# Kernel optimization log

Hardware: AMD Instinct MI355X
Metric: run time of the kernel (lower is better)

The kernel has to match this reference:

```python
import jax, jax.numpy as jnp
import numpy as np

NUM_HEADS = 16
HEAD_DIM = 128
HIDDEN = NUM_HEADS * HEAD_DIM


def rotate_half(x):
    x1, x2 = jnp.split(x, 2, axis=-1)
    return jnp.concatenate((-x2, x1), axis=-1)


def setup_inputs() -> dict:
    key = jax.random.key(0)
    ks = jax.random.split(key, 7)
    b, s = 2, 2048
    return {
        "hidden_states": jax.random.normal(ks[0], (b, s, HIDDEN), dtype=jnp.float32),
        "cos": jax.random.normal(ks[1], (1, 1, s, HEAD_DIM), dtype=jnp.float32),
        "sin": jax.random.normal(ks[2], (1, 1, s, HEAD_DIM), dtype=jnp.float32),
        "Wq": jax.random.normal(ks[3], (HIDDEN, HIDDEN), dtype=jnp.float32) * 0.02,
        "Wk": jax.random.normal(ks[4], (HIDDEN, HIDDEN), dtype=jnp.float32) * 0.02,
        "Wv": jax.random.normal(ks[5], (HIDDEN, HIDDEN), dtype=jnp.float32) * 0.02,
        "Wo": jax.random.normal(ks[6], (HIDDEN, HIDDEN), dtype=jnp.float32) * 0.02,
    }


def reference(hidden_states, cos, sin, Wq, Wk, Wv, Wo):
    b, s, _ = hidden_states.shape

    def proj(W):
        # [b,s,hidden] -> [b,H,s,D]
        return (hidden_states @ W).reshape(b, s, NUM_HEADS, HEAD_DIM).transpose(0, 2, 1, 3)

    q = proj(Wq)
    k = proj(Wk)
    v = proj(Wv)

    # RoPE: cos/sin [1,1,s,D] broadcast over batch and heads
    q = q * cos + rotate_half(q) * sin
    k = k * cos + rotate_half(k) * sin

    scale = 1.0 / jnp.sqrt(jnp.asarray(HEAD_DIM, dtype=q.dtype))
    scores = jnp.einsum("bhqd,bhkd->bhqk", q, k) * scale  # [b,H,s,s]
    attn = jax.nn.softmax(scores, axis=-1)  # no mask applied (matches source)
    out = jnp.einsum("bhqk,bhkd->bhqd", attn, v)  # [b,H,s,D]
    out = out.transpose(0, 2, 1, 3).reshape(b, s, HIDDEN)
    return out @ Wo
```

## Files before the change

### kernel.cpp

```cpp
#include <hip/hip_runtime.h>

typedef short bf16x8 __attribute__((ext_vector_type(8)));
typedef float f32x4 __attribute__((ext_vector_type(4)));

#define HID   2048
#define S_LEN 2048
#define NH    16
#define HD    128
#define BATCH 2
#define NROWS (BATCH * S_LEN)

__device__ __forceinline__ float bf2f(unsigned short u) {
    union { unsigned int i; float f; } v;
    v.i = ((unsigned int)u) << 16;
    return v.f;
}
__device__ __forceinline__ unsigned short f2bf(float f) {
    union { float f; unsigned int i; } v;
    v.f = f;
    unsigned int u = v.i;
    return (unsigned short)((u + 0x7fffu + ((u >> 16) & 1u)) >> 16);
}

__device__ __forceinline__ unsigned int pkbf(float a, float b) {
#if defined(__has_builtin) && __has_builtin(__builtin_amdgcn_cvt_pk_bf16_f32)
    typedef __bf16 bf2_t __attribute__((ext_vector_type(2)));
    bf2_t v = __builtin_amdgcn_cvt_pk_bf16_f32(a, b);
    unsigned int u;
    __builtin_memcpy(&u, &v, 4);
    return u;
#else
    return (unsigned int)f2bf(a) | ((unsigned int)f2bf(b) << 16);
#endif
}

__device__ __forceinline__ float exp2_fast(float x) {
#if defined(__has_builtin) && __has_builtin(__builtin_amdgcn_exp2f)
    return __builtin_amdgcn_exp2f(x);
#else
    return __expf(x * 0.6931471805599453f);
#endif
}

__device__ __forceinline__ void async16(const unsigned short* g, unsigned short* l) {
    __builtin_amdgcn_global_load_lds(
        (const __attribute__((address_space(1))) unsigned int*)g,
        (__attribute__((address_space(3))) unsigned int*)l, 16, 0, 0);
}

__global__ __launch_bounds__(256) void prep(const float* __restrict__ hs,
                                            const float* __restrict__ Wa,
                                            const float* __restrict__ Wb,
                                            const float* __restrict__ Wc,
                                            unsigned short* __restrict__ Xb,
                                            unsigned short* __restrict__ WT) {
    int z = blockIdx.z;
    int t = threadIdx.x;
    if (z == 3) {
        size_t idx = (((size_t)blockIdx.y * 64 + blockIdx.x) * 256 + t) * 8;
        float4 v0 = *(const float4*)(hs + idx);
        float4 v1 = *(const float4*)(hs + idx + 4);
        uint4 o;
        o.x = pkbf(v0.x, v0.y);
        o.y = pkbf(v0.z, v0.w);
        o.z = pkbf(v1.x, v1.y);
        o.w = pkbf(v1.z, v1.w);
        *(uint4*)(Xb + idx) = o;
        return;
    }
    __shared__ float tile[32][33];
    int tx = t & 31, ty = t >> 5;
    int bx = blockIdx.x, by = blockIdx.y;
    const float* W = (z == 0) ? Wa : ((z == 1) ? Wb : Wc);
    unsigned short* dst = WT + (size_t)z * HID * HID;
#pragma unroll
    for (int i = 0; i < 4; i++)
        tile[ty + i * 8][tx] = W[(size_t)(by * 32 + ty + i * 8) * HID + bx * 32 + tx];
    __syncthreads();
#pragma unroll
    for (int i = 0; i < 4; i++)
        dst[(size_t)(bx * 32 + ty + i * 8) * HID + by * 32 + tx] = f2bf(tile[tx][ty + i * 8]);
}

__global__ __launch_bounds__(256) void transpose_cast(const float* __restrict__ W,
                                                      unsigned short* __restrict__ WT) {
    __shared__ float tile[32][33];
    int t = threadIdx.x;
    int tx = t & 31, ty = t >> 5;
    int bx = blockIdx.x, by = blockIdx.y;
#pragma unroll
    for (int i = 0; i < 4; i++)
        tile[ty + i * 8][tx] = W[(size_t)(by * 32 + ty + i * 8) * HID + bx * 32 + tx];
    __syncthreads();
#pragma unroll
    for (int i = 0; i < 4; i++)
        WT[(size_t)(bx * 32 + ty + i * 8) * HID + by * 32 + tx] = f2bf(tile[tx][ty + i * 8]);
}

template <int MODE>
__global__ __launch_bounds__(256, 2) void gemm_bt(const unsigned short* __restrict__ A,
                                                  const unsigned short* __restrict__ Bt,
                                                  unsigned short* __restrict__ Qo,
                                                  unsigned short* __restrict__ Ko,
                                                  unsigned short* __restrict__ Vo,
                                                  float* __restrict__ Fo,
                                                  const float* __restrict__ cosp,
                                                  const float* __restrict__ sinp,
                                                  int n_shift) {
    __shared__ unsigned short SM[16384];
    unsigned short* Asm = SM;
    unsigned short* Bsm = SM + 8192;
    int t = threadIdx.x;
    int wave = t >> 6, lane = t & 63;
    int wm = wave >> 1, wn = wave & 1;
    int c = lane & 15, quad = lane >> 4;
    int m0 = blockIdx.y * 128, nloc = blockIdx.x * 128;

    int lr = lane >> 3;
    int cb = (lane & 7) ^ (lr & 7);
    const unsigned short* Ag = A + (size_t)(m0 + wave * 32 + lr) * HID + cb * 8;
    const unsigned short* Bg = Bt + (size_t)(nloc + wave * 32 + lr) * HID + cb * 8;
    unsigned short* Al = Asm + wave * 2048;
    unsigned short* Bl = Bsm + wave * 2048;

    f32x4 zero = {0.f, 0.f, 0.f, 0.f};
    f32x4 acc[4][4];
#pragma unroll
    for (int i = 0; i < 4; i++)
#pragma unroll
        for (int j = 0; j < 4; j++) acc[i][j] = zero;

    for (int it = 0; it < 32; it++) {
        int k0 = it * 64;
#pragma unroll
        for (int j = 0; j < 4; j++) {
            async16(Ag + k0 + j * 8 * HID, Al + j * 512);
            async16(Bg + k0 + j * 8 * HID, Bl + j * 512);
        }
        __syncthreads();
#pragma unroll
        for (int kk = 0; kk < 2; kk++) {
            bf16x8 af[4], bfr[4];
#pragma unroll
            for (int mt = 0; mt < 4; mt++)
                af[mt] = *(const bf16x8*)(Asm + (wm * 64 + mt * 16 + c) * 64 +
                                          (((kk * 4 + quad) ^ (c & 7)) * 8));
#pragma unroll
            for (int nt = 0; nt < 4; nt++)
                bfr[nt] = *(const bf16x8*)(Bsm + (wn * 64 + nt * 16 + c) * 64 +
                                           (((kk * 4 + quad) ^ (c & 7)) * 8));
#pragma unroll
            for (int mt = 0; mt < 4; mt++)
#pragma unroll
                for (int nt = 0; nt < 4; nt++)
                    acc[mt][nt] = __builtin_amdgcn_mfma_f32_16x16x32_bf16(af[mt], bfr[nt],
                                                                          acc[mt][nt], 0, 0, 0);
        }
        __syncthreads();
    }

    if (MODE == 2) {
#pragma unroll
        for (int mt = 0; mt < 4; mt++)
#pragma unroll
            for (int nt = 0; nt < 4; nt++)
#pragma unroll
                for (int r = 0; r < 4; r++) {
                    int row = m0 + wm * 64 + mt * 16 + quad * 4 + r;
                    int col = nloc + wn * 64 + nt * 16 + c;
                    Fo[(size_t)row * HID + col] = acc[mt][nt][r];
                }
    } else {
        int nglob0 = n_shift + nloc;
        int mat = nglob0 >> 11;
        int h = (nglob0 & 2047) >> 7;
        if (mat == 2) {
#pragma unroll
            for (int mt = 0; mt < 4; mt++)
#pragma unroll
                for (int nt = 0; nt < 4; nt++) {
                    int d = wn * 64 + nt * 16 + c;
                    int row0 = m0 + wm * 64 + mt * 16 + quad * 4;
                    int b = row0 >> 11, s = row0 & 2047;
                    ushort4 o;
                    o.x = f2bf(acc[mt][nt][0]);
                    o.y = f2bf(acc[mt][nt][1]);
                    o.z = f2bf(acc[mt][nt][2]);
                    o.w = f2bf(acc[mt][nt][3]);
                    *(ushort4*)(Vo + ((size_t)(b * NH + h) * HD + d) * S_LEN + s) = o;
                }
        } else {
            unsigned short* Cb = (mat == 0) ? Qo : Ko;
            float scl = (mat == 0) ? 0.12751743f : 1.0f;
            __syncthreads();
#pragma unroll
            for (int mt = 0; mt < 4; mt++)
#pragma unroll
                for (int nt = 0; nt < 4; nt++) {
                    ushort4 o;
                    o.x = f2bf(acc[mt][nt][0]);
                    o.y = f2bf(acc[mt][nt][1]);
                    o.z = f2bf(acc[mt][nt][2]);
                    o.w = f2bf(acc[mt][nt][3]);
                    *(ushort4*)(SM + (mt * 4 + nt) * 1024 + t * 4) = o;
                }
            __syncthreads();
            int partner = (wm * 2 + (wn ^ 1)) * 64 + lane;
            float sgn = wn ? 1.0f : -1.0f;
#pragma unroll
            for (int mt = 0; mt < 4; mt++) {
#pragma unroll
                for (int nt = 0; nt < 4; nt++) {
                    ushort4 pv = *(const ushort4*)(SM + (mt * 4 + nt) * 1024 + partner * 4);
                    float part[4] = {bf2f(pv.x), bf2f(pv.y), bf2f(pv.z), bf2f(pv.w)};
                    int col = wn * 64 + nt * 16 + c;
#pragma unroll
                    for (int r = 0; r < 4; r++) {
                        int row = m0 + wm * 64 + mt * 16 + quad * 4 + r;
                        int b = row >> 11, s = row & 2047;
                        float cv = cosp[s * HD + col], sv = sinp[s * HD + col];
                        float out = (acc[mt][nt][r] * cv + sgn * part[r] * sv) * scl;
                        Cb[((size_t)(b * NH + h) * S_LEN + s) * HD + col] = f2bf(out);
                    }
                }
            }
        }
    }
}

#define PKS 72
__global__ __launch_bounds__(256, 2) void attn_kernel(const unsigned short* __restrict__ Q,
                                                      const unsigned short* __restrict__ Kg,
                                                      const unsigned short* __restrict__ Vt,
                                                      unsigned short* __restrict__ Aout) {
    __shared__ unsigned short Ksm[64 * 128];
    __shared__ unsigned short Vsm[128 * 64];
    __shared__ __align__(16) unsigned short Psm[4 * 2 * 16 * PKS];
    int bh = blockIdx.y;
    int b = bh >> 4, h = bh & 15;
    int t = threadIdx.x;
    int wave = t >> 6, lane = t & 63;
    int c = lane & 15, quad = lane >> 4;
    int q0 = blockIdx.x * 128 + wave * 32;
    const unsigned short* Qp = Q + (size_t)bh * S_LEN * HD;
    const unsigned short* Kp = Kg + (size_t)bh * S_LEN * HD;
    const unsigned short* Vp = Vt + (size_t)bh * HD * S_LEN;

    bf16x8 qf[2][4];
#pragma unroll
    for (int qn = 0; qn < 2; qn++)
#pragma unroll
        for (int kk = 0; kk < 4; kk++)
            qf[qn][kk] = *(const bf16x8*)(Qp + (size_t)(q0 + qn * 16 + c) * HD + kk * 32 + quad * 8);

    f32x4 zero = {0.f, 0.f, 0.f, 0.f};
    f32x4 o_acc[2][8];
#pragma unroll
    for (int qn = 0; qn < 2; qn++)
#pragma unroll
        for (int nt = 0; nt < 8; nt++) o_acc[qn][nt] = zero;
    float lsum[2] = {0.f, 0.f};

    for (int key0 = 0; key0 < S_LEN; key0 += 64) {
#pragma unroll
        for (int j = 0; j < 4; j++) {
            int fc = (wave * 4 + j) * 64 + lane;
            int rK = fc >> 4, cbK = (fc & 15) ^ (rK & 15);
            async16(Kp + (size_t)(key0 + rK) * HD + cbK * 8, Ksm + (wave * 4 + j) * 512);
            int rV = fc >> 3, cbV = (fc & 7) ^ (rV & 7);
            async16(Vp + (size_t)rV * S_LEN + key0 + cbV * 8, Vsm + (wave * 4 + j) * 512);
        }
        __syncthreads();

        f32x4 sacc[4][2];
#pragma unroll
        for (int km = 0; km < 4; km++)
#pragma unroll
            for (int qn = 0; qn < 2; qn++) sacc[km][qn] = zero;
#pragma unroll
        for (int kk = 0; kk < 4; kk++) {
            bf16x8 kfr[4];
#pragma unroll
            for (int km = 0; km < 4; km++)
                kfr[km] = *(const bf16x8*)(Ksm + (km * 16 + c) * HD + (((kk * 4 + quad) ^ c)) * 8);
#pragma unroll
            for (int km = 0; km < 4; km++)
#pragma unroll
                for (int qn = 0; qn < 2; qn++)
                    sacc[km][qn] = __builtin_amdgcn_mfma_f32_16x16x32_bf16(kfr[km], qf[qn][kk],
                                                                           sacc[km][qn], 0, 0, 0);
        }

#pragma unroll
        for (int qn = 0; qn < 2; qn++) {
#pragma unroll
            for (int km = 0; km < 4; km++) {
                float e0 = exp2_fast(sacc[km][qn][0]);
                float e1 = exp2_fast(sacc[km][qn][1]);
                float e2 = exp2_fast(sacc[km][qn][2]);
                float e3 = exp2_fast(sacc[km][qn][3]);
                lsum[qn] += (e0 + e1) + (e2 + e3);
                uint2 pk;
                pk.x = pkbf(e0, e1);
                pk.y = pkbf(e2, e3);
                *(uint2*)(Psm + ((wave * 2 + qn) * 16 + c) * PKS + km * 16 + quad * 4) = pk;
            }
        }
        asm volatile("" ::: "memory");
        __builtin_amdgcn_s_waitcnt(0xc07f);
        asm volatile("" ::: "memory");

#pragma unroll
        for (int kf = 0; kf < 2; kf++) {
            bf16x8 pf[2];
#pragma unroll
            for (int qn = 0; qn < 2; qn++)
                pf[qn] = *(const bf16x8*)(Psm + ((wave * 2 + qn) * 16 + c) * PKS + kf * 32 + quad * 8);
#pragma unroll
            for (int nt = 0; nt < 8; nt++) {
                bf16x8 vf = *(const bf16x8*)(Vsm + (nt * 16 + c) * 64 +
                                             (((kf * 4 + quad) ^ (c & 7))) * 8);
#pragma unroll
                for (int qn = 0; qn < 2; qn++)
                    o_acc[qn][nt] = __builtin_amdgcn_mfma_f32_16x16x32_bf16(pf[qn], vf,
                                                                            o_acc[qn][nt], 0, 0, 0);
            }
        }
        __syncthreads();
    }

#pragma unroll
    for (int qn = 0; qn < 2; qn++) {
        lsum[qn] += __shfl_xor(lsum[qn], 16);
        lsum[qn] += __shfl_xor(lsum[qn], 32);
    }
    float inv[2][4];
#pragma unroll
    for (int qn = 0; qn < 2; qn++)
#pragma unroll
        for (int r = 0; r < 4; r++)
            inv[qn][r] = 1.0f / __shfl(lsum[qn], quad * 4 + r);

#pragma unroll
    for (int qn = 0; qn < 2; qn++) {
#pragma unroll
        for (int r = 0; r < 4; r++) {
            int srow = q0 + qn * 16 + quad * 4 + r;
            size_t base = ((size_t)(b * S_LEN + srow)) * HID + h * HD;
#pragma unroll
            for (int nt = 0; nt < 8; nt++)
                Aout[base + nt * 16 + c] = f2bf(o_acc[qn][nt][r] * inv[qn][r]);
        }
    }
}

extern "C" void kernel_launch(void* const* d_in, const int* in_sizes, int n_in,
                              void* d_out, int out_size, void* d_ws, size_t ws_size,
                              hipStream_t stream) {
    const float* hs   = (const float*)d_in[0];
    const float* cosp = (const float*)d_in[1];
    const float* sinp = (const float*)d_in[2];
    const float* Wq   = (const float*)d_in[3];
    const float* Wk   = (const float*)d_in[4];
    const float* Wv   = (const float*)d_in[5];
    const float* Wo   = (const float*)d_in[6];

    char* ws = (char*)d_ws;
    unsigned short* Xb = (unsigned short*)(ws);
    unsigned short* Qb = (unsigned short*)(ws + (16ull << 20));
    unsigned short* Kb = (unsigned short*)(ws + (32ull << 20));
    unsigned short* Vb = (unsigned short*)(ws + (48ull << 20));
    unsigned short* WT = (unsigned short*)(ws + (64ull << 20));

    const bool fused = ws_size >= (88ull << 20);

    if (fused) {
        prep<<<dim3(64, 64, 4), 256, 0, stream>>>(hs, Wq, Wk, Wv, Xb, WT);
        gemm_bt<0><<<dim3(48, 32), 256, 0, stream>>>(Xb, WT, Qb, Kb, Vb, nullptr,
                                                     cosp, sinp, 0);
        attn_kernel<<<dim3(16, 32), 256, 0, stream>>>(Qb, Kb, Vb, Xb );
        unsigned short* WoT = (unsigned short*)(ws + (16ull << 20));
        transpose_cast<<<dim3(64, 64), 256, 0, stream>>>(Wo, WoT);
        gemm_bt<2><<<dim3(16, 32), 256, 0, stream>>>(Xb, WoT, nullptr, nullptr, nullptr,
                                                     (float*)d_out, cosp, sinp, 0);
    } else {
        prep<<<dim3(64, 64, 1), 256, 0, stream>>>(hs, Wq, Wq, Wq, Xb, WT);
        prep<<<dim3(64, 64, 4), 256, 0, stream>>>(hs, Wq, Wq, Wq, Xb, WT);
        gemm_bt<0><<<dim3(16, 32), 256, 0, stream>>>(Xb, WT, Qb, Kb, Vb, nullptr,
                                                     cosp, sinp, 0);
        transpose_cast<<<dim3(64, 64), 256, 0, stream>>>(Wk, WT);
        gemm_bt<0><<<dim3(16, 32), 256, 0, stream>>>(Xb, WT, Qb, Kb, Vb, nullptr,
                                                     cosp, sinp, 2048);
        transpose_cast<<<dim3(64, 64), 256, 0, stream>>>(Wv, WT);
        gemm_bt<0><<<dim3(16, 32), 256, 0, stream>>>(Xb, WT, Qb, Kb, Vb, nullptr,
                                                     cosp, sinp, 4096);
        attn_kernel<<<dim3(16, 32), 256, 0, stream>>>(Qb, Kb, Vb, Xb );
        transpose_cast<<<dim3(64, 64), 256, 0, stream>>>(Wo, WT);
        gemm_bt<2><<<dim3(16, 32), 256, 0, stream>>>(Xb, WT, nullptr, nullptr, nullptr,
                                                     (float*)d_out, cosp, sinp, 0);
    }
}
```

Measured before the change: 400.7 us.

## Add 256x256-tile QKV projection GEMM with multi-stage async LDS pipeline

Replaces the 128x128-tile fused QKV projection GEMM with a new 512-thread kernel that computes 256x256 output tiles. It uses a four-slot LDS ring filled by async global-to-LDS copies two k-steps ahead, and splits each k-step into two MFMA phases interleaved with loads under barriers and raised wave priority. The RoPE/scale and V-transpose epilogue is kept, with the rotate-half partner exchanged through LDS. Larger tiles cut global and LDS traffic per FLOP, but only 384 blocks with 128 KB of LDS each may leave CUs unevenly loaded and limit occupancy.

```diff
diff --git a/kernel.cpp b/kernel.cpp
--- a/kernel.cpp
+++ b/kernel.cpp
@@ -97,6 +97,147 @@
         WT[(size_t)(bx * 32 + ty + i * 8) * HID + by * 32 + tx] = f2bf(tile[tx][ty + i * 8]);
 }
 
+__global__ __launch_bounds__(512, 2) void gemm256(const unsigned short* __restrict__ A,
+                                                  const unsigned short* __restrict__ Bt,
+                                                  unsigned short* __restrict__ Qo,
+                                                  unsigned short* __restrict__ Ko,
+                                                  unsigned short* __restrict__ Vo,
+                                                  const float* __restrict__ cosp,
+                                                  const float* __restrict__ sinp) {
+    __shared__ unsigned short SM[65536];
+    int t = threadIdx.x;
+    int wave = t >> 6, lane = t & 63;
+    int wm = wave >> 2, wn = wave & 3;
+    int c = lane & 15, quad = lane >> 4;
+    int m0 = blockIdx.y * 256, n0 = blockIdx.x * 256;
+
+    int lr = wave * 16 + (lane >> 2);
+    int scw = ((lane & 3) ^ ((lane >> 2) & 3)) * 8;
+    const unsigned short* Ag = A + (size_t)(m0 + lr) * HID + scw;
+    const unsigned short* Bg = Bt + (size_t)(n0 + lr) * HID + scw;
+
+    f32x4 zero = {0.f, 0.f, 0.f, 0.f};
+    f32x4 acc[8][4];
+#pragma unroll
+    for (int i = 0; i < 8; i++)
+#pragma unroll
+        for (int j = 0; j < 4; j++) acc[i][j] = zero;
+
+#pragma unroll
+    for (int kt = 0; kt < 2; kt++) {
+        unsigned short* Sl = SM + kt * 16384;
+        async16(Ag + kt * 32, Sl + wave * 512);
+        async16(Ag + kt * 32 + 128 * HID, Sl + wave * 512 + 4096);
+        async16(Bg + kt * 32, Sl + 8192 + wave * 512);
+        async16(Bg + kt * 32 + 128 * HID, Sl + 8192 + wave * 512 + 4096);
+    }
+    __builtin_amdgcn_s_waitcnt(0x0F74);
+    __builtin_amdgcn_s_barrier();
+
+    int cxor = (quad ^ (c & 3)) * 8;
+
+#pragma unroll 4
+    for (int kt = 0; kt < 64; kt++) {
+        const unsigned short* Sa = SM + (kt & 3) * 16384;
+        const unsigned short* Sb = Sa + 8192;
+        int ktn = (kt + 2 > 63) ? 63 : kt + 2;
+        unsigned short* Sn = SM + (ktn & 3) * 16384;
+
+        async16(Ag + ktn * 32, Sn + wave * 512);
+        async16(Ag + ktn * 32 + 128 * HID, Sn + wave * 512 + 4096);
+        bf16x8 af[4], bfr[4];
+#pragma unroll
+        for (int mt = 0; mt < 4; mt++)
+            af[mt] = *(const bf16x8*)(Sa + (wm * 128 + mt * 16 + c) * 32 + cxor);
+#pragma unroll
+        for (int nt = 0; nt < 4; nt++)
+            bfr[nt] = *(const bf16x8*)(Sb + (wn * 64 + nt * 16 + c) * 32 + cxor);
+        __builtin_amdgcn_s_barrier();
+        __builtin_amdgcn_s_setprio(1);
+#pragma unroll
+        for (int mt = 0; mt < 4; mt++)
+#pragma unroll
+            for (int nt = 0; nt < 4; nt++)
+                acc[mt][nt] = __builtin_amdgcn_mfma_f32_16x16x32_bf16(af[mt], bfr[nt],
+                                                                      acc[mt][nt], 0, 0, 0);
+        __builtin_amdgcn_s_setprio(0);
+        __builtin_amdgcn_s_barrier();
+
+        async16(Bg + ktn * 32, Sn + 8192 + wave * 512);
+        async16(Bg + ktn * 32 + 128 * HID, Sn + 8192 + wave * 512 + 4096);
+#pragma unroll
+        for (int mt = 0; mt < 4; mt++)
+            af[mt] = *(const bf16x8*)(Sa + (wm * 128 + (mt + 4) * 16 + c) * 32 + cxor);
+        __builtin_amdgcn_s_waitcnt(0x0F74);
+        __builtin_amdgcn_s_barrier();
+        __builtin_amdgcn_s_setprio(1);
+#pragma unroll
+        for (int mt = 0; mt < 4; mt++)
+#pragma unroll
+            for (int nt = 0; nt < 4; nt++)
+                acc[mt + 4][nt] = __builtin_amdgcn_mfma_f32_16x16x32_bf16(af[mt], bfr[nt],
+                                                                          acc[mt + 4][nt], 0, 0, 0);
+        __builtin_amdgcn_s_setprio(0);
+        __builtin_amdgcn_s_barrier();
+    }
+
+    __syncthreads();
+
+    int mat = n0 >> 11;
+    int hbase = (n0 & 2047) >> 7;
+    int h = hbase + (wn >> 1);
+    if (mat == 2) {
+#pragma unroll
+        for (int mt = 0; mt < 8; mt++)
+#pragma unroll
+            for (int nt = 0; nt < 4; nt++) {
+                int d = (wn & 1) * 64 + nt * 16 + c;
+                int row0 = m0 + wm * 128 + mt * 16 + quad * 4;
+                int b = row0 >> 11, s = row0 & 2047;
+                ushort4 o;
+                o.x = f2bf(acc[mt][nt][0]);
+                o.y = f2bf(acc[mt][nt][1]);
+                o.z = f2bf(acc[mt][nt][2]);
+                o.w = f2bf(acc[mt][nt][3]);
+                *(ushort4*)(Vo + ((size_t)(b * NH + h) * HD + d) * S_LEN + s) = o;
+            }
+    } else {
+        unsigned short* Cb = (mat == 0) ? Qo : Ko;
+        float scl = (mat == 0) ? 0.12751743f : 1.0f;
+#pragma unroll
+        for (int mt = 0; mt < 8; mt++)
+#pragma unroll
+            for (int nt = 0; nt < 4; nt++) {
+                ushort4 o;
+                o.x = f2bf(acc[mt][nt][0]);
+                o.y = f2bf(acc[mt][nt][1]);
+                o.z = f2bf(acc[mt][nt][2]);
+                o.w = f2bf(acc[mt][nt][3]);
+                *(ushort4*)(SM + (mt * 4 + nt) * 2048 + t * 4) = o;
+            }
+        __syncthreads();
+        int partner = (wave ^ 1) * 64 + lane;
+        float sgn = (wn & 1) ? 1.0f : -1.0f;
+#pragma unroll
+        for (int mt = 0; mt < 8; mt++) {
+#pragma unroll
+            for (int nt = 0; nt < 4; nt++) {
+                ushort4 pv = *(const ushort4*)(SM + (mt * 4 + nt) * 2048 + partner * 4);
+                float part[4] = {bf2f(pv.x), bf2f(pv.y), bf2f(pv.z), bf2f(pv.w)};
+                int d = (wn & 1) * 64 + nt * 16 + c;
+#pragma unroll
+                for (int r = 0; r < 4; r++) {
+                    int row = m0 + wm * 128 + mt * 16 + quad * 4 + r;
+                    int b = row >> 11, s = row & 2047;
+                    float cv = cosp[s * HD + d], sv = sinp[s * HD + d];
+                    float out = (acc[mt][nt][r] * cv + sgn * part[r] * sv) * scl;
+                    Cb[((size_t)(b * NH + h) * S_LEN + s) * HD + d] = f2bf(out);
+                }
+            }
+        }
+    }
+}
+
 template <int MODE>
 __global__ __launch_bounds__(256, 2) void gemm_bt(const unsigned short* __restrict__ A,
                                                   const unsigned short* __restrict__ Bt,
@@ -376,8 +517,7 @@
 
     if (fused) {
         prep<<<dim3(64, 64, 4), 256, 0, stream>>>(hs, Wq, Wk, Wv, Xb, WT);
-        gemm_bt<0><<<dim3(48, 32), 256, 0, stream>>>(Xb, WT, Qb, Kb, Vb, nullptr,
-                                                     cosp, sinp, 0);
+        gemm256<<<dim3(24, 16), 512, 0, stream>>>(Xb, WT, Qb, Kb, Vb, cosp, sinp);
         attn_kernel<<<dim3(16, 32), 256, 0, stream>>>(Qb, Kb, Vb, Xb );
         unsigned short* WoT = (unsigned short*)(ws + (16ull << 20));
         transpose_cast<<<dim3(64, 64), 256, 0, stream>>>(Wo, WoT);
```

New measurement: 451.6 us. +12.7%, slower.

## Double-buffer K tiles and prefetch next K/V chunks with vmcnt-gated barriers

Applied to the files above, without the earlier changes.

The attention loop now keeps two K buffers in LDS and issues async loads for the next V chunk and the K chunk two steps ahead at the end of each iteration. Partial vmcnt waits let the QK^T MFMAs start once only the current K has landed, and the PV stage waits separately for V. This overlaps global-to-LDS transfers with compute instead of stalling on a full sync per tile. The cost is an extra 16KB of LDS per block, which may reduce occupancy under the launch bound of two blocks, plus redundant clamped loads in the last iterations.

```diff
diff --git a/kernel.cpp b/kernel.cpp
--- a/kernel.cpp
+++ b/kernel.cpp
@@ -233,7 +233,7 @@
                                                       const unsigned short* __restrict__ Kg,
                                                       const unsigned short* __restrict__ Vt,
                                                       unsigned short* __restrict__ Aout) {
-    __shared__ unsigned short Ksm[64 * 128];
+    __shared__ unsigned short Ksm[2 * 64 * 128];
     __shared__ unsigned short Vsm[128 * 64];
     __shared__ __align__(16) unsigned short Psm[4 * 2 * 16 * PKS];
     int bh = blockIdx.y;
@@ -261,16 +261,30 @@
         for (int nt = 0; nt < 8; nt++) o_acc[qn][nt] = zero;
     float lsum[2] = {0.f, 0.f};
 
-    for (int key0 = 0; key0 < S_LEN; key0 += 64) {
-#pragma unroll
-        for (int j = 0; j < 4; j++) {
-            int fc = (wave * 4 + j) * 64 + lane;
-            int rK = fc >> 4, cbK = (fc & 15) ^ (rK & 15);
-            async16(Kp + (size_t)(key0 + rK) * HD + cbK * 8, Ksm + (wave * 4 + j) * 512);
-            int rV = fc >> 3, cbV = (fc & 7) ^ (rV & 7);
-            async16(Vp + (size_t)rV * S_LEN + key0 + cbV * 8, Vsm + (wave * 4 + j) * 512);
-        }
-        __syncthreads();
+#define STAGE_K(CH, BUF) {                                                      \
+    _Pragma("unroll")                                                           \
+    for (int j = 0; j < 4; j++) {                                               \
+        int fc = (wave * 4 + j) * 64 + lane;                                    \
+        int rK = fc >> 4, cbK = (fc & 15) ^ (rK & 15);                          \
+        async16(Kp + (size_t)((CH) * 64 + rK) * HD + cbK * 8,                   \
+                Ksm + (BUF) * 8192 + (wave * 4 + j) * 512); } }
+#define STAGE_V(CH) {                                                           \
+    _Pragma("unroll")                                                           \
+    for (int j = 0; j < 4; j++) {                                               \
+        int fc = (wave * 4 + j) * 64 + lane;                                    \
+        int rV = fc >> 3, cbV = (fc & 7) ^ (rV & 7);                            \
+        async16(Vp + (size_t)rV * S_LEN + (CH) * 64 + cbV * 8,                  \
+                Vsm + (wave * 4 + j) * 512); } }
+
+    STAGE_K(0, 0);
+    STAGE_V(0);
+    STAGE_K(1, 1);
+
+    for (int i = 0; i < 32; i++) {
+        const unsigned short* Kb = Ksm + (i & 1) * 8192;
+        __builtin_amdgcn_s_waitcnt(0x0F78);
+        __builtin_amdgcn_s_barrier();
+        __builtin_amdgcn_sched_barrier(0);
 
         f32x4 sacc[4][2];
 #pragma unroll
@@ -282,7 +296,7 @@
             bf16x8 kfr[4];
 #pragma unroll
             for (int km = 0; km < 4; km++)
-                kfr[km] = *(const bf16x8*)(Ksm + (km * 16 + c) * HD + (((kk * 4 + quad) ^ c)) * 8);
+                kfr[km] = *(const bf16x8*)(Kb + (km * 16 + c) * HD + (((kk * 4 + quad) ^ c)) * 8);
 #pragma unroll
             for (int km = 0; km < 4; km++)
 #pragma unroll
@@ -310,6 +324,11 @@
         __builtin_amdgcn_s_waitcnt(0xc07f);
         asm volatile("" ::: "memory");
 
+        __builtin_amdgcn_sched_barrier(0);
+        __builtin_amdgcn_s_waitcnt(0x0F74);
+        __builtin_amdgcn_s_barrier();
+        __builtin_amdgcn_sched_barrier(0);
+
 #pragma unroll
         for (int kf = 0; kf < 2; kf++) {
             bf16x8 pf[2];
@@ -326,8 +345,17 @@
                                                                             o_acc[qn][nt], 0, 0, 0);
             }
         }
-        __syncthreads();
-    }
+        __builtin_amdgcn_sched_barrier(0);
+        __builtin_amdgcn_s_barrier();
+        __builtin_amdgcn_sched_barrier(0);
+
+        int nv = (i + 1 > 31) ? 31 : i + 1;
+        int nk = (i + 2 > 31) ? 31 : i + 2;
+        STAGE_V(nv);
+        STAGE_K(nk, (i & 1));
+    }
+#undef STAGE_K
+#undef STAGE_V
 
 #pragma unroll
     for (int qn = 0; qn < 2; qn++) {
```

Measured after the change: 387.8 us. 3.2% less time.
